# Kernel optimization log

Hardware: AMD Instinct MI355X
Metric: run time of the kernel (lower is better)

Reference implementation:

```python
import jax, jax.numpy as jnp
import numpy as np

B, N, DIN, HID = 64, 1024, 128, 128
NEG = 9000000000000000.0


def setup_inputs() -> dict:
    key = jax.random.key(0)
    ks = jax.random.split(key, 8)
    s = 1.0 / np.sqrt(DIN)
    x = jax.random.normal(ks[0], (B, N, DIN), dtype=jnp.float32)
    mask = jax.random.randint(ks[1], (B, N, N), 0, 2, dtype=jnp.int32)
    Wv = jax.random.uniform(ks[2], (HID, DIN), jnp.float32, -s, s)
    bv = jax.random.uniform(ks[3], (HID,), jnp.float32, -s, s)
    Wk = jax.random.uniform(ks[4], (HID, DIN), jnp.float32, -s, s)
    bk = jax.random.uniform(ks[5], (HID,), jnp.float32, -s, s)
    Wq = jax.random.uniform(ks[6], (HID, DIN), jnp.float32, -s, s)
    bq = jax.random.uniform(ks[7], (HID,), jnp.float32, -s, s)
    return {"x": x, "mask": mask, "Wv": Wv, "bv": bv, "Wk": Wk, "bk": bk, "Wq": Wq, "bq": bq}


def reference(x, mask, Wv, bv, Wk, bk, Wq, bq):
    m = mask.astype(x.dtype)                       # [B,N,N]
    v = jnp.tanh(jnp.einsum('bnd,hd->bnh', x, Wv) + bv)  # [B,N,H]
    q = jnp.tanh(jnp.einsum('bnd,hd->bnh', x, Wq) + bq)
    k = jnp.tanh(jnp.einsum('bnd,hd->bnh', x, Wk) + bk)
    scores = jnp.einsum('bih,bjh->bij', q, k)      # bmm(q, k^T)
    att = jax.nn.softmax(scores * m - NEG * (1.0 - m), axis=2)
    out = jnp.einsum('bij,bjh->bih', att, v)       # [B,N,H]
    return out
```

## Files before the change

kernel.cpp:

```cpp
#include <hip/hip_runtime.h>
#include <cstdint>
#include <cstddef>

#define BB 64
#define NN 1024
#define DD 128

typedef short    bf16x8 __attribute__((ext_vector_type(8)));
typedef _Float16 f16x8  __attribute__((ext_vector_type(8)));
typedef float    f32x4  __attribute__((ext_vector_type(4)));

__device__ __forceinline__ unsigned short f2bf(float f) {
  union { float f; unsigned u; } v; v.f = f;
  unsigned r = v.u + 0x7FFFu + ((v.u >> 16) & 1u);
  return (unsigned short)(r >> 16);
}
__device__ __forceinline__ unsigned short f2h(float f) {
  union { _Float16 h; unsigned short u; } v; v.h = (_Float16)f;
  return v.u;
}
__device__ __forceinline__ float fast_tanh(float x) {
  x = fminf(15.0f, fmaxf(-15.0f, x));
  float e = __expf(2.0f * x);
  return (e - 1.0f) / (e + 1.0f);
}

__device__ __forceinline__ void async_copy16(void* lptr, const void* gptr) {
  __builtin_amdgcn_global_load_lds(
      (const __attribute__((address_space(1))) unsigned int*)gptr,
      (__attribute__((address_space(3))) unsigned int*)lptr, 16, 0, 0);
}

__device__ __forceinline__ unsigned pack_mask(const int4 m[4]) {
  unsigned mb = 0;
#pragma unroll
  for (int i = 0; i < 4; ++i) {
    mb |= (unsigned)(m[i].x & 1) << (i * 4 + 0);
    mb |= (unsigned)(m[i].y & 1) << (i * 4 + 1);
    mb |= (unsigned)(m[i].z & 1) << (i * 4 + 2);
    mb |= (unsigned)(m[i].w & 1) << (i * 4 + 3);
  }
  return mb;
}

__global__ __launch_bounds__(256, 2) void proj_kernel(
    const float* __restrict__ x,
    const float* __restrict__ Wq, const float* __restrict__ bq,
    const float* __restrict__ Wk, const float* __restrict__ bk,
    const float* __restrict__ Wv, const float* __restrict__ bv,
    unsigned short* __restrict__ qg,
    unsigned short* __restrict__ kg,
    unsigned short* __restrict__ vtg)
{
  __shared__ unsigned short wlds[128 * 136];

  const int tid  = threadIdx.x;
  const int lane = tid & 63;
  const int wave = tid >> 6;
  const int quad = lane >> 4;
  const int mr   = lane & 15;
  const int m0   = blockIdx.x * 128;
  const int batch = m0 >> 10;
  const int n0    = m0 & 1023;

  bf16x8 xa[2][4];
#pragma unroll
  for (int mt = 0; mt < 2; ++mt) {
    const float* xr = x + (size_t)(m0 + wave * 32 + mt * 16 + mr) * DD + quad * 8;
#pragma unroll
    for (int ks = 0; ks < 4; ++ks) {
      const float4* xp = (const float4*)(xr + ks * 32);
      float4 f0 = xp[0], f1 = xp[1];
      bf16x8 f;
      f[0] = (short)f2bf(f0.x); f[1] = (short)f2bf(f0.y);
      f[2] = (short)f2bf(f0.z); f[3] = (short)f2bf(f0.w);
      f[4] = (short)f2bf(f1.x); f[5] = (short)f2bf(f1.y);
      f[6] = (short)f2bf(f1.z); f[7] = (short)f2bf(f1.w);
      xa[mt][ks] = f;
    }
  }

  const float* Wp[3] = {Wq, Wk, Wv};
  const float* bp[3] = {bq, bk, bv};

  for (int w = 0; w < 3; ++w) {
    __syncthreads();
    {
      const int row = tid >> 1, half = tid & 1;
      const float* src = Wp[w] + row * 128 + half * 64;
      unsigned short* dst = wlds + row * 136 + half * 64;
#pragma unroll
      for (int c = 0; c < 64; c += 8) {
        const float4* sp = (const float4*)(src + c);
        float4 f0 = sp[0], f1 = sp[1];
        unsigned short tmp[8];
        tmp[0] = f2bf(f0.x); tmp[1] = f2bf(f0.y); tmp[2] = f2bf(f0.z); tmp[3] = f2bf(f0.w);
        tmp[4] = f2bf(f1.x); tmp[5] = f2bf(f1.y); tmp[6] = f2bf(f1.z); tmp[7] = f2bf(f1.w);
        uint4 pk; __builtin_memcpy(&pk, tmp, 16);
        *(uint4*)(dst + c) = pk;
      }
    }
    __syncthreads();

    f32x4 z = {0.f, 0.f, 0.f, 0.f};
    f32x4 acc[2][8];
#pragma unroll
    for (int mt = 0; mt < 2; ++mt)
#pragma unroll
      for (int nt = 0; nt < 8; ++nt) acc[mt][nt] = z;

#pragma unroll
    for (int ks = 0; ks < 4; ++ks) {
#pragma unroll
      for (int nt = 0; nt < 8; ++nt) {
        bf16x8 bfr = *(const bf16x8*)(wlds + (nt * 16 + mr) * 136 + ks * 32 + quad * 8);
        acc[0][nt] = __builtin_amdgcn_mfma_f32_16x16x32_bf16(xa[0][ks], bfr, acc[0][nt], 0, 0, 0);
        acc[1][nt] = __builtin_amdgcn_mfma_f32_16x16x32_bf16(xa[1][ks], bfr, acc[1][nt], 0, 0, 0);
      }
    }

    if (w < 2) {
      unsigned short* outg = (w == 0) ? qg : kg;
#pragma unroll
      for (int mt = 0; mt < 2; ++mt) {
        const int rowbase = m0 + wave * 32 + mt * 16 + quad * 4;
#pragma unroll
        for (int nt = 0; nt < 8; ++nt) {
          float bb = bp[w][nt * 16 + mr];
#pragma unroll
          for (int r = 0; r < 4; ++r) {
            float t = fast_tanh(acc[mt][nt][r] + bb);
            outg[(size_t)(rowbase + r) * DD + nt * 16 + mr] = f2h(t);
          }
        }
      }
    } else {
      __syncthreads();
#pragma unroll
      for (int mt = 0; mt < 2; ++mt) {
        const int ib = wave * 32 + mt * 16 + quad * 4;
#pragma unroll
        for (int nt = 0; nt < 8; ++nt) {
          float bb = bp[2][nt * 16 + mr];
#pragma unroll
          for (int r = 0; r < 4; ++r) {
            float t = fast_tanh(acc[mt][nt][r] + bb);
            wlds[(nt * 16 + mr) * 136 + ib + r] = f2bf(t);
          }
        }
      }
      __syncthreads();
      const int h = tid >> 1, half = tid & 1;
      const unsigned short* src = wlds + h * 136 + half * 64;
      unsigned short* dst = vtg + (size_t)(batch * 128 + h) * NN + n0 + half * 64;
#pragma unroll
      for (int c = 0; c < 64; c += 8)
        *(uint4*)(dst + c) = *(const uint4*)(src + c);
    }
  }
}

__global__ __launch_bounds__(256, 4) void attn_kernel(
    const unsigned short* __restrict__ qg,
    const unsigned short* __restrict__ kg,
    const unsigned short* __restrict__ vtg,
    const int* __restrict__ mask,
    float* __restrict__ out)
{
  extern __shared__ unsigned short lds[];
  unsigned short* klds = lds;
  unsigned short* plds = lds;
  unsigned short* vlds = lds + 8192;

  const int tid  = threadIdx.x;
  const int lane = tid & 63;
  const int wave = tid >> 6;
  const int quad = lane >> 4;
  const int mr   = lane & 15;

  const int bx    = blockIdx.x;
  const int batch = ((bx >> 7) << 3) | (bx & 7);
  const int i0    = ((bx >> 3) & 15) * 64;

  const unsigned short* kgb = kg  + (size_t)batch * NN * DD;
  const unsigned short* vtb = vtg + (size_t)batch * DD * NN;
  const int* mrow = mask + ((size_t)batch << 20) + (size_t)(i0 + wave * 16 + mr) * NN;

  f16x8 qa[4];
#pragma unroll
  for (int ks = 0; ks < 4; ++ks)
    qa[ks] = *(const f16x8*)(qg +
        ((size_t)batch * NN + i0 + wave * 16 + mr) * DD + ks * 32 + quad * 8);

  f32x4 z = {0.f, 0.f, 0.f, 0.f};
  f32x4 o[8];
#pragma unroll
  for (int nt = 0; nt < 8; ++nt) o[nt] = z;
  float rowsum = 0.0f;

  unsigned mb;
  {
    int4 mreg[4];
    mreg[0] = *(const int4*)(mrow + quad * 8);
    mreg[1] = *(const int4*)(mrow + quad * 8 + 4);
    mreg[2] = *(const int4*)(mrow + 32 + quad * 8);
    mreg[3] = *(const int4*)(mrow + 32 + quad * 8 + 4);
    mb = pack_mask(mreg);
  }

  for (int t = 0; t < 16; ++t) {
    const int j0 = t * 64;

    __syncthreads();
#pragma unroll
    for (int p = 0; p < 4; ++p) {
      int s = p * 256 + tid;
      int kr = s >> 4, kgp = (s & 15) ^ (kr & 15);
      async_copy16(klds + s * 8, kgb + (size_t)(j0 + kr) * DD + kgp * 8);
    }
#pragma unroll
    for (int p = 0; p < 4; ++p) {
      int s = p * 256 + tid;
      int vr = s >> 3, vgp = (s & 7) ^ (vr & 7);
      async_copy16(vlds + s * 8, vtb + (size_t)vr * NN + j0 + vgp * 8);
    }
    __syncthreads();

    int4 mreg[4];
    {
      const int j0n = ((t + 1) & 15) * 64;
      mreg[0] = *(const int4*)(mrow + j0n + quad * 8);
      mreg[1] = *(const int4*)(mrow + j0n + quad * 8 + 4);
      mreg[2] = *(const int4*)(mrow + j0n + 32 + quad * 8);
      mreg[3] = *(const int4*)(mrow + j0n + 32 + quad * 8 + 4);
    }

    f32x4 s[4];
#pragma unroll
    for (int nt = 0; nt < 4; ++nt) s[nt] = z;
    __builtin_amdgcn_s_setprio(1);
#pragma unroll
    for (int ks = 0; ks < 4; ++ks) {
#pragma unroll
      for (int nt = 0; nt < 4; ++nt) {
        f16x8 kb = *(const f16x8*)(klds + (nt * 16 + mr) * 128 + (((ks * 4 + quad) ^ mr) * 8));
        s[nt] = __builtin_amdgcn_mfma_f32_16x16x32_f16(qa[ks], kb, s[nt], 0, 0, 0);
      }
    }
    __builtin_amdgcn_s_setprio(0);

    unsigned mb_next = pack_mask(mreg);

    __syncthreads();

#pragma unroll
    for (int nt = 0; nt < 4; ++nt) {
#pragma unroll
      for (int r = 0; r < 4; ++r)
        plds[(wave * 16 + quad * 4 + r) * 72 + nt * 16 + mr] = f2bf(__expf(s[nt][r]));
    }

#pragma unroll
    for (int ks2 = 0; ks2 < 2; ++ks2) {
      bf16x8 pa = *(const bf16x8*)(plds + (wave * 16 + mr) * 72 + ks2 * 32 + quad * 8);
      bf16x8 pm;
#pragma unroll
      for (int e = 0; e < 8; ++e) {
        unsigned bit = (mb >> (ks2 * 8 + e)) & 1u;
        short pv = bit ? pa[e] : (short)0;
        pm[e] = pv;
        union { unsigned u; float f; } cv;
        cv.u = ((unsigned)(unsigned short)pv) << 16;
        rowsum += cv.f;
      }
      __builtin_amdgcn_s_setprio(1);
#pragma unroll
      for (int nt = 0; nt < 8; ++nt) {
        bf16x8 vb = *(const bf16x8*)(vlds + (nt * 16 + mr) * 64 +
                                     (((ks2 * 4 + quad) ^ (mr & 7)) * 8));
        o[nt] = __builtin_amdgcn_mfma_f32_16x16x32_bf16(pm, vb, o[nt], 0, 0, 0);
      }
      __builtin_amdgcn_s_setprio(0);
    }

    mb = mb_next;
  }

  rowsum += __shfl_xor(rowsum, 16, 64);
  rowsum += __shfl_xor(rowsum, 32, 64);

  float* ob = out + ((size_t)batch * NN + i0) * DD;
#pragma unroll
  for (int r = 0; r < 4; ++r) {
    float rs  = __shfl(rowsum, quad * 4 + r, 64);
    float inv = 1.0f / rs;
    float* orow = ob + (size_t)(wave * 16 + quad * 4 + r) * DD + mr;
#pragma unroll
    for (int nt = 0; nt < 8; ++nt)
      orow[nt * 16] = o[nt][r] * inv;
  }
}

extern "C" void kernel_launch(void* const* d_in, const int* in_sizes, int n_in,
                              void* d_out, int out_size, void* d_ws, size_t ws_size,
                              hipStream_t stream) {
  (void)in_sizes; (void)n_in; (void)out_size; (void)ws_size;
  const float* x  = (const float*)d_in[0];
  const int* mask = (const int*)d_in[1];
  const float* Wv = (const float*)d_in[2];
  const float* bv = (const float*)d_in[3];
  const float* Wk = (const float*)d_in[4];
  const float* bk = (const float*)d_in[5];
  const float* Wq = (const float*)d_in[6];
  const float* bq = (const float*)d_in[7];
  float* out = (float*)d_out;

  unsigned short* qg  = (unsigned short*)d_ws;
  unsigned short* kg  = qg + (size_t)BB * NN * DD;
  unsigned short* vtg = kg + (size_t)BB * NN * DD;

  proj_kernel<<<512, 256, 0, stream>>>(x, Wq, bq, Wk, bk, Wv, bv, qg, kg, vtg);
  attn_kernel<<<1024, 256, 32768, stream>>>(qg, kg, vtg, mask, out);
}
```

Measured before the change: 458.6 us.

## Double-buffer K/V tiles in LDS and compute row sums via MFMA

```diff
diff --git a/kernel.cpp b/kernel.cpp
--- a/kernel.cpp
+++ b/kernel.cpp
@@ -160,7 +160,7 @@
   }
 }
 
-__global__ __launch_bounds__(256, 4) void attn_kernel(
+__global__ __launch_bounds__(256, 2) void attn_kernel(
     const unsigned short* __restrict__ qg,
     const unsigned short* __restrict__ kg,
     const unsigned short* __restrict__ vtg,
@@ -168,9 +168,6 @@
     float* __restrict__ out)
 {
   extern __shared__ unsigned short lds[];
-  unsigned short* klds = lds;
-  unsigned short* plds = lds;
-  unsigned short* vlds = lds + 8192;
 
   const int tid  = threadIdx.x;
   const int lane = tid & 63;
@@ -196,34 +193,42 @@
   f32x4 o[8];
 #pragma unroll
   for (int nt = 0; nt < 8; ++nt) o[nt] = z;
-  float rowsum = 0.0f;
-
-  unsigned mb;
+  f32x4 rs = z;
+  bf16x8 ones;
+#pragma unroll
+  for (int e = 0; e < 8; ++e) ones[e] = (short)0x3F80;
+
+  int4 mreg0[4];
+  mreg0[0] = *(const int4*)(mrow + quad * 8);
+  mreg0[1] = *(const int4*)(mrow + quad * 8 + 4);
+  mreg0[2] = *(const int4*)(mrow + 32 + quad * 8);
+  mreg0[3] = *(const int4*)(mrow + 32 + quad * 8 + 4);
+
   {
-    int4 mreg[4];
-    mreg[0] = *(const int4*)(mrow + quad * 8);
-    mreg[1] = *(const int4*)(mrow + quad * 8 + 4);
-    mreg[2] = *(const int4*)(mrow + 32 + quad * 8);
-    mreg[3] = *(const int4*)(mrow + 32 + quad * 8 + 4);
-    mb = pack_mask(mreg);
-  }
-
-  for (int t = 0; t < 16; ++t) {
-    const int j0 = t * 64;
-
-    __syncthreads();
+    unsigned short* klds0 = lds;
+    unsigned short* vlds0 = lds + 8192;
 #pragma unroll
     for (int p = 0; p < 4; ++p) {
       int s = p * 256 + tid;
       int kr = s >> 4, kgp = (s & 15) ^ (kr & 15);
-      async_copy16(klds + s * 8, kgb + (size_t)(j0 + kr) * DD + kgp * 8);
+      async_copy16(klds0 + s * 8, kgb + (size_t)kr * DD + kgp * 8);
     }
 #pragma unroll
     for (int p = 0; p < 4; ++p) {
       int s = p * 256 + tid;
       int vr = s >> 3, vgp = (s & 7) ^ (vr & 7);
-      async_copy16(vlds + s * 8, vtb + (size_t)vr * NN + j0 + vgp * 8);
-    }
+      async_copy16(vlds0 + s * 8, vtb + (size_t)vr * NN + vgp * 8);
+    }
+  }
+
+  unsigned mb = pack_mask(mreg0);
+
+  int cur = 0;
+  for (int t = 0; t < 16; ++t) {
+    unsigned short* klds_c = lds + cur * 16384;
+    unsigned short* vlds_c = lds + cur * 16384 + 8192;
+    unsigned short* plds_c = klds_c;
+
     __syncthreads();
 
     int4 mreg[4];
@@ -235,6 +240,24 @@
       mreg[3] = *(const int4*)(mrow + j0n + 32 + quad * 8 + 4);
     }
 
+    if (t < 15) {
+      unsigned short* klds_n = lds + (cur ^ 1) * 16384;
+      unsigned short* vlds_n = lds + (cur ^ 1) * 16384 + 8192;
+      const int j0s = (t + 1) * 64;
+#pragma unroll
+      for (int p = 0; p < 4; ++p) {
+        int s = p * 256 + tid;
+        int kr = s >> 4, kgp = (s & 15) ^ (kr & 15);
+        async_copy16(klds_n + s * 8, kgb + (size_t)(j0s + kr) * DD + kgp * 8);
+      }
+#pragma unroll
+      for (int p = 0; p < 4; ++p) {
+        int s = p * 256 + tid;
+        int vr = s >> 3, vgp = (s & 7) ^ (vr & 7);
+        async_copy16(vlds_n + s * 8, vtb + (size_t)vr * NN + j0s + vgp * 8);
+      }
+    }
+
     f32x4 s[4];
 #pragma unroll
     for (int nt = 0; nt < 4; ++nt) s[nt] = z;
@@ -243,7 +266,7 @@
     for (int ks = 0; ks < 4; ++ks) {
 #pragma unroll
       for (int nt = 0; nt < 4; ++nt) {
-        f16x8 kb = *(const f16x8*)(klds + (nt * 16 + mr) * 128 + (((ks * 4 + quad) ^ mr) * 8));
+        f16x8 kb = *(const f16x8*)(klds_c + (nt * 16 + mr) * 128 + (((ks * 4 + quad) ^ mr) * 8));
         s[nt] = __builtin_amdgcn_mfma_f32_16x16x32_f16(qa[ks], kb, s[nt], 0, 0, 0);
       }
     }
@@ -251,32 +274,30 @@
 
     unsigned mb_next = pack_mask(mreg);
 
-    __syncthreads();
+    asm volatile("s_waitcnt lgkmcnt(0)" ::: "memory");
+    __builtin_amdgcn_s_barrier();
 
 #pragma unroll
     for (int nt = 0; nt < 4; ++nt) {
 #pragma unroll
       for (int r = 0; r < 4; ++r)
-        plds[(wave * 16 + quad * 4 + r) * 72 + nt * 16 + mr] = f2bf(__expf(s[nt][r]));
+        plds_c[(wave * 16 + quad * 4 + r) * 72 + nt * 16 + mr] = f2bf(__expf(s[nt][r]));
     }
 
 #pragma unroll
     for (int ks2 = 0; ks2 < 2; ++ks2) {
-      bf16x8 pa = *(const bf16x8*)(plds + (wave * 16 + mr) * 72 + ks2 * 32 + quad * 8);
+      bf16x8 pa = *(const bf16x8*)(plds_c + (wave * 16 + mr) * 72 + ks2 * 32 + quad * 8);
       bf16x8 pm;
 #pragma unroll
       for (int e = 0; e < 8; ++e) {
         unsigned bit = (mb >> (ks2 * 8 + e)) & 1u;
-        short pv = bit ? pa[e] : (short)0;
-        pm[e] = pv;
-        union { unsigned u; float f; } cv;
-        cv.u = ((unsigned)(unsigned short)pv) << 16;
-        rowsum += cv.f;
-      }
+        pm[e] = bit ? pa[e] : (short)0;
+      }
+      rs = __builtin_amdgcn_mfma_f32_16x16x32_bf16(pm, ones, rs, 0, 0, 0);
       __builtin_amdgcn_s_setprio(1);
 #pragma unroll
       for (int nt = 0; nt < 8; ++nt) {
-        bf16x8 vb = *(const bf16x8*)(vlds + (nt * 16 + mr) * 64 +
+        bf16x8 vb = *(const bf16x8*)(vlds_c + (nt * 16 + mr) * 64 +
                                      (((ks2 * 4 + quad) ^ (mr & 7)) * 8));
         o[nt] = __builtin_amdgcn_mfma_f32_16x16x32_bf16(pm, vb, o[nt], 0, 0, 0);
       }
@@ -284,16 +305,13 @@
     }
 
     mb = mb_next;
-  }
-
-  rowsum += __shfl_xor(rowsum, 16, 64);
-  rowsum += __shfl_xor(rowsum, 32, 64);
+    cur ^= 1;
+  }
 
   float* ob = out + ((size_t)batch * NN + i0) * DD;
 #pragma unroll
   for (int r = 0; r < 4; ++r) {
-    float rs  = __shfl(rowsum, quad * 4 + r, 64);
-    float inv = 1.0f / rs;
+    float inv = 1.0f / rs[r];
     float* orow = ob + (size_t)(wave * 16 + quad * 4 + r) * DD + mr;
 #pragma unroll
     for (int nt = 0; nt < 8; ++nt)
@@ -320,5 +338,5 @@
   unsigned short* vtg = kg + (size_t)BB * NN * DD;
 
   proj_kernel<<<512, 256, 0, stream>>>(x, Wq, bq, Wk, bk, Wv, bv, qg, kg, vtg);
-  attn_kernel<<<1024, 256, 32768, stream>>>(qg, kg, vtg, mask, out);
-}
+  attn_kernel<<<1024, 256, 65536, stream>>>(qg, kg, vtg, mask, out);
+}
```

Result: slower. 478.4 us (+4.3%).

## Double attention block to 128 rows, give P its own LDS region, compute rowsum via MFMA

Applied to the files above, without the earlier changes.

```diff
diff --git a/kernel.cpp b/kernel.cpp
--- a/kernel.cpp
+++ b/kernel.cpp
@@ -160,7 +160,7 @@
   }
 }
 
-__global__ __launch_bounds__(256, 4) void attn_kernel(
+__global__ __launch_bounds__(512, 4) void attn_kernel(
     const unsigned short* __restrict__ qg,
     const unsigned short* __restrict__ kg,
     const unsigned short* __restrict__ vtg,
@@ -169,8 +169,8 @@
 {
   extern __shared__ unsigned short lds[];
   unsigned short* klds = lds;
-  unsigned short* plds = lds;
   unsigned short* vlds = lds + 8192;
+  unsigned short* plds = lds + 16384;
 
   const int tid  = threadIdx.x;
   const int lane = tid & 63;
@@ -179,8 +179,8 @@
   const int mr   = lane & 15;
 
   const int bx    = blockIdx.x;
-  const int batch = ((bx >> 7) << 3) | (bx & 7);
-  const int i0    = ((bx >> 3) & 15) * 64;
+  const int batch = ((bx >> 6) << 3) | (bx & 7);
+  const int i0    = ((bx >> 3) & 7) * 128;
 
   const unsigned short* kgb = kg  + (size_t)batch * NN * DD;
   const unsigned short* vtb = vtg + (size_t)batch * DD * NN;
@@ -196,34 +196,39 @@
   f32x4 o[8];
 #pragma unroll
   for (int nt = 0; nt < 8; ++nt) o[nt] = z;
-  float rowsum = 0.0f;
+  f32x4 rs = z;
+  bf16x8 ones;
+#pragma unroll
+  for (int e = 0; e < 8; ++e) ones[e] = (short)0x3F80;
 
   unsigned mb;
   {
-    int4 mreg[4];
-    mreg[0] = *(const int4*)(mrow + quad * 8);
-    mreg[1] = *(const int4*)(mrow + quad * 8 + 4);
-    mreg[2] = *(const int4*)(mrow + 32 + quad * 8);
-    mreg[3] = *(const int4*)(mrow + 32 + quad * 8 + 4);
-    mb = pack_mask(mreg);
+    int4 m0r[4];
+    m0r[0] = *(const int4*)(mrow + quad * 8);
+    m0r[1] = *(const int4*)(mrow + quad * 8 + 4);
+    m0r[2] = *(const int4*)(mrow + 32 + quad * 8);
+    m0r[3] = *(const int4*)(mrow + 32 + quad * 8 + 4);
+    mb = pack_mask(m0r);
   }
 
   for (int t = 0; t < 16; ++t) {
     const int j0 = t * 64;
 
     __syncthreads();
-#pragma unroll
-    for (int p = 0; p < 4; ++p) {
-      int s = p * 256 + tid;
+
+#pragma unroll
+    for (int p = 0; p < 2; ++p) {
+      int s = p * 512 + tid;
       int kr = s >> 4, kgp = (s & 15) ^ (kr & 15);
       async_copy16(klds + s * 8, kgb + (size_t)(j0 + kr) * DD + kgp * 8);
     }
 #pragma unroll
-    for (int p = 0; p < 4; ++p) {
-      int s = p * 256 + tid;
+    for (int p = 0; p < 2; ++p) {
+      int s = p * 512 + tid;
       int vr = s >> 3, vgp = (s & 7) ^ (vr & 7);
       async_copy16(vlds + s * 8, vtb + (size_t)vr * NN + j0 + vgp * 8);
     }
+
     __syncthreads();
 
     int4 mreg[4];
@@ -249,10 +254,6 @@
     }
     __builtin_amdgcn_s_setprio(0);
 
-    unsigned mb_next = pack_mask(mreg);
-
-    __syncthreads();
-
 #pragma unroll
     for (int nt = 0; nt < 4; ++nt) {
 #pragma unroll
@@ -267,12 +268,9 @@
 #pragma unroll
       for (int e = 0; e < 8; ++e) {
         unsigned bit = (mb >> (ks2 * 8 + e)) & 1u;
-        short pv = bit ? pa[e] : (short)0;
-        pm[e] = pv;
-        union { unsigned u; float f; } cv;
-        cv.u = ((unsigned)(unsigned short)pv) << 16;
-        rowsum += cv.f;
-      }
+        pm[e] = bit ? pa[e] : (short)0;
+      }
+      rs = __builtin_amdgcn_mfma_f32_16x16x32_bf16(pm, ones, rs, 0, 0, 0);
       __builtin_amdgcn_s_setprio(1);
 #pragma unroll
       for (int nt = 0; nt < 8; ++nt) {
@@ -283,17 +281,13 @@
       __builtin_amdgcn_s_setprio(0);
     }
 
-    mb = mb_next;
-  }
-
-  rowsum += __shfl_xor(rowsum, 16, 64);
-  rowsum += __shfl_xor(rowsum, 32, 64);
+    mb = pack_mask(mreg);
+  }
 
   float* ob = out + ((size_t)batch * NN + i0) * DD;
 #pragma unroll
   for (int r = 0; r < 4; ++r) {
-    float rs  = __shfl(rowsum, quad * 4 + r, 64);
-    float inv = 1.0f / rs;
+    float inv = 1.0f / rs[r];
     float* orow = ob + (size_t)(wave * 16 + quad * 4 + r) * DD + mr;
 #pragma unroll
     for (int nt = 0; nt < 8; ++nt)
@@ -320,5 +314,5 @@
   unsigned short* vtg = kg + (size_t)BB * NN * DD;
 
   proj_kernel<<<512, 256, 0, stream>>>(x, Wq, bq, Wk, bk, Wv, bv, qg, kg, vtg);
-  attn_kernel<<<1024, 256, 32768, stream>>>(qg, kg, vtg, mask, out);
-}
+  attn_kernel<<<512, 512, 51200, stream>>>(qg, kg, vtg, mask, out);
+}
```

After: 456.8 us. Within noise of the previous version (-0.4%).
